# Kernel optimization log

Measured on AMD Instinct MI355X. Metric: run time of the kernel, lower is better.

The kernel has to match this reference:

```python
import jax, jax.numpy as jnp
import numpy as np

B, L, D, H = 2, 1024, 1024, 16
HEAD = D // H
BUCKETS = 256
MAX_REL = 512
ATT_SPAN = BUCKETS          # pos_ebd_size = position_buckets when buckets > 0
SCALE_FACTOR = 3            # 1 (content) + 1 (c2p) + 1 (p2c)


def _log_bucket(rel, bucket_size, max_position):
    """make_log_bucket_position: signed log-bucketed relative positions."""
    sign = jnp.sign(rel).astype(jnp.float32)
    mid = bucket_size // 2
    abs_pos = jnp.where((rel < mid) & (rel > -mid), mid - 1, jnp.abs(rel)).astype(jnp.float32)
    log_pos = jnp.ceil(jnp.log(abs_pos / mid) / np.float32(np.log((max_position - 1) / mid)) * (mid - 1)) + mid
    bucket = jnp.where(abs_pos <= mid, rel.astype(jnp.float32), log_pos * sign)
    return bucket.astype(jnp.int32)


def build_relative_position(q_len, k_len):
    rel = jnp.arange(q_len, dtype=jnp.int32)[:, None] - jnp.arange(k_len, dtype=jnp.int32)[None, :]
    return _log_bucket(rel, BUCKETS, MAX_REL)  # [q_len, k_len]


def setup_inputs() -> dict:
    key = jax.random.key(0)
    ks = jax.random.split(key, 6)
    w = 0.02  # typical init scale, keeps softmax well-conditioned
    return {
        "hidden_states": jax.random.normal(ks[0], (B, L, D), jnp.float32),
        "attention_mask": jnp.ones((B, L), jnp.int32),
        "rel_embeddings": jax.random.normal(ks[1], (2 * ATT_SPAN, D), jnp.float32) * w,
        "Wq": jax.random.normal(ks[2], (D, D), jnp.float32) * w,
        "bq": jnp.zeros((D,), jnp.float32),
        "Wk": jax.random.normal(ks[3], (D, D), jnp.float32) * w,
        "bk": jnp.zeros((D,), jnp.float32),
        "Wv": jax.random.normal(ks[4], (D, D), jnp.float32) * w,
        "bv": jnp.zeros((D,), jnp.float32),
    }


def reference(hidden_states, attention_mask, rel_embeddings, Wq, bq, Wk, bk, Wv, bv):
    Bn, Ln, Dn = hidden_states.shape

    def proj(x, W, b):  # Linear with bias, torch convention y = x W^T + b
        return x @ W.T + b

    def to_heads(x):  # [.., L, D] -> [.., H, L, HEAD]
        return x.reshape(*x.shape[:-1], H, HEAD).swapaxes(-3, -2)

    q = to_heads(proj(hidden_states, Wq, bq))  # [B,H,L,d]
    k = to_heads(proj(hidden_states, Wk, bk))
    v = to_heads(proj(hidden_states, Wv, bv))

    scale = jnp.sqrt(jnp.float32(HEAD * SCALE_FACTOR))
    scores = jnp.einsum('bhqd,bhkd->bhqk', q, k) / scale

    # disentangled relative-position bias (share_att_key=True -> reuse Wq/Wk)
    rel = build_relative_position(Ln, Ln)                     # [L,L] log-bucketed
    pos_k = proj(rel_embeddings, Wk, bk).reshape(2 * ATT_SPAN, H, HEAD)
    pos_q = proj(rel_embeddings, Wq, bq).reshape(2 * ATT_SPAN, H, HEAD)

    # c2p: Q . posK, gathered at (rel + span)
    c2p_att = jnp.einsum('bhqd,phd->bhqp', q, pos_k)          # [B,H,L,2S]
    c2p_idx = jnp.clip(rel + ATT_SPAN, 0, 2 * ATT_SPAN - 1)   # [L,L]
    c2p = jnp.take_along_axis(c2p_att, jnp.broadcast_to(c2p_idx[None, None], (Bn, H, Ln, Ln)), axis=-1)

    # p2c: K . posQ gathered at (-rel + span), then transposed to [q,k]
    p2c_att = jnp.einsum('bhkd,phd->bhkp', k, pos_q)          # [B,H,L,2S]
    p2c_idx = jnp.clip(-rel + ATT_SPAN, 0, 2 * ATT_SPAN - 1)
    p2c = jnp.take_along_axis(p2c_att, jnp.broadcast_to(p2c_idx[None, None], (Bn, H, Ln, Ln)), axis=-1)
    p2c = jnp.swapaxes(p2c, -1, -2)

    scores = scores + (c2p + p2c) / scale

    bias = jnp.where(attention_mask[:, None, None, :] > 0, 0.0, -1e9).astype(scores.dtype)
    probs = jax.nn.softmax(scores + bias, axis=-1)
    ctx = jnp.einsum('bhqk,bhkd->bhqd', probs, v)
    return ctx.swapaxes(1, 2).reshape(Bn, Ln, Dn)
```

## Files before the change

kernel.cpp:

```cpp
#include <hip/hip_runtime.h>


typedef short s8v __attribute__((ext_vector_type(8)));
typedef short s4v __attribute__((ext_vector_type(4)));
typedef float f32x4 __attribute__((ext_vector_type(4)));
typedef float f4v __attribute__((ext_vector_type(4)));

#define QK_SCALE 0.26864243f

__device__ __forceinline__ unsigned short f2bf(float f) {
  unsigned u = __builtin_bit_cast(unsigned, f);
  u += 0x7fffu + ((u >> 16) & 1u);
  return (unsigned short)(u >> 16);
}
__device__ __forceinline__ float bf2f(unsigned short h) {
  unsigned u = ((unsigned)h) << 16;
  return __builtin_bit_cast(float, u);
}

__device__ __forceinline__ void gload_lds16(const void* g, void* l) {
  __builtin_amdgcn_global_load_lds(
      (const __attribute__((address_space(1))) void*)g,
      (__attribute__((address_space(3))) void*)l, 16, 0, 0);
}

__global__ __launch_bounds__(256) void prep_kernel(
    const float* __restrict__ hidden, const float* __restrict__ rel,
    const float* __restrict__ Wq, const float* __restrict__ Wk,
    const float* __restrict__ Wv, const int* __restrict__ mask,
    short* __restrict__ Abf, short* __restrict__ Wbf,
    float* __restrict__ mbias, short* __restrict__ Tt) {
  int idx = blockIdx.x * 256 + threadIdx.x;
  const int NCONV = 1441792;
  if (idx < NCONV) {
    const float* src; short* dst; int off;
    if (idx < 524288) { src = hidden; dst = Abf; off = idx; }
    else if (idx < 655360) { src = rel; dst = Abf + 2048 * 1024; off = idx - 524288; }
    else {
      int j = idx - 655360;
      int w = j / 262144; off = j - w * 262144;
      src = (w == 0) ? Wq : (w == 1) ? Wk : Wv;
      dst = Wbf + w * 1048576;
    }
    f4v v = ((const f4v*)src)[off];
    s4v o;
    o[0] = (short)f2bf(v[0]); o[1] = (short)f2bf(v[1]);
    o[2] = (short)f2bf(v[2]); o[3] = (short)f2bf(v[3]);
    ((s4v*)dst)[off] = o;
  } else {
    int j = idx - NCONV;
    if (j < 2047) {
      int r = j - 1023;
      float fr = (float)r;
      float sign = (r > 0) ? 1.f : ((r < 0) ? -1.f : 0.f);
      float abs_pos = (r < 128 && r > -128) ? 127.f : fabsf(fr);
      const float logc = 1.3843393245589053f;
      float log_pos = ceilf(logf(abs_pos * (1.f / 128.f)) / logc * 127.f) + 128.f;
      float bucket = (abs_pos <= 128.f) ? fr : log_pos * sign;
      int bi = (int)bucket + 256;
      bi = bi < 0 ? 0 : (bi > 511 ? 511 : bi);
      Tt[j] = (short)bi;
    } else if (j < 4095) {
      int m = j - 2047;
      mbias[m] = (mask[m] > 0) ? 0.f : -1e9f;
    }
  }
}

__global__ __launch_bounds__(256) void gemm_qkv(
    const short* __restrict__ Abf, const short* __restrict__ Wbf,
    const float* __restrict__ bq, const float* __restrict__ bk,
    const float* __restrict__ bv,
    short* __restrict__ Qc, short* __restrict__ Kc, short* __restrict__ Vc) {
  __shared__ short As[128 * 64];
  __shared__ short Bs[128 * 64];
  int tid = threadIdx.x;
  int wid = tid >> 6, lane = tid & 63;
  int lr = lane & 15, lg = lane >> 4;
  int wr = wid >> 1, wc = wid & 1;
  int z = blockIdx.z;
  const short* W = Wbf + z * 1048576;
  const float* bias = (z == 0) ? bq : (z == 1) ? bk : bv;
  short* C = (z == 0) ? Qc : (z == 1) ? Kc : Vc;
  float scale = (z == 2) ? 1.f : QK_SCALE;
  int brow = blockIdx.y * 128;
  int bcol = blockIdx.x * 128;

  f32x4 acc[4][4];
  for (int i = 0; i < 4; i++)
    for (int j = 0; j < 4; j++) acc[i][j] = (f32x4){0.f, 0.f, 0.f, 0.f};

  for (int k0 = 0; k0 < 1024; k0 += 64) {
    for (int i = 0; i < 4; i++) {
      int n = i * 256 + wid * 64 + lane;
      const short* gA = Abf + (size_t)(brow + (n >> 3)) * 1024 + k0 + (n & 7) * 8;
      gload_lds16(gA, &As[(i * 256 + wid * 64) * 8]);
      const short* gB = W + (size_t)(bcol + (n >> 3)) * 1024 + k0 + (n & 7) * 8;
      gload_lds16(gB, &Bs[(i * 256 + wid * 64) * 8]);
    }
    __syncthreads();
    for (int ks = 0; ks < 2; ks++) {
      s8v af[4], bfv[4];
      for (int mi = 0; mi < 4; mi++)
        af[mi] = *(const s8v*)&As[(wr * 64 + mi * 16 + lr) * 64 + ks * 32 + lg * 8];
      for (int ni = 0; ni < 4; ni++)
        bfv[ni] = *(const s8v*)&Bs[(wc * 64 + ni * 16 + lr) * 64 + ks * 32 + lg * 8];
      for (int mi = 0; mi < 4; mi++)
        for (int ni = 0; ni < 4; ni++)
          acc[mi][ni] = __builtin_amdgcn_mfma_f32_16x16x32_bf16(
              af[mi], bfv[ni], acc[mi][ni], 0, 0, 0);
    }
    __syncthreads();
  }
  for (int mi = 0; mi < 4; mi++)
    for (int ni = 0; ni < 4; ni++) {
      int col = bcol + wc * 64 + ni * 16 + lr;
      float bb = bias[col];
      for (int r = 0; r < 4; r++) {
        int row = brow + wr * 64 + mi * 16 + lg * 4 + r;
        float v = (acc[mi][ni][r] + bb) * scale;
        C[(size_t)row * 1024 + col] = (short)f2bf(v);
      }
    }
}

__global__ __launch_bounds__(256) void pos_gemm(
    const short* __restrict__ Qc, const short* __restrict__ Kc,
    short* __restrict__ c2p, short* __restrict__ p2c) {
  __shared__ short As[128 * 64];
  __shared__ short Bs[128 * 64];
  int tid = threadIdx.x;
  int wid = tid >> 6, lane = tid & 63;
  int lr = lane & 15, lg = lane >> 4;
  int wr = wid >> 1, wc = wid & 1;
  int zz = blockIdx.z;
  int which = zz >> 5;
  int bh = zz & 31;
  int b = bh >> 4, h = bh & 15;
  const short* Arows = (which == 0) ? Qc : Kc;
  const short* Brows = (which == 0) ? Kc : Qc;
  short* Out = (which == 0) ? c2p : p2c;
  int mrow = blockIdx.y * 128;
  int ncol = blockIdx.x * 128;

  for (int i = 0; i < 4; i++) {
    int n = i * 256 + wid * 64 + lane;
    const short* gA = Arows + (size_t)(b * 1024 + mrow + (n >> 3)) * 1024 + h * 64 + (n & 7) * 8;
    gload_lds16(gA, &As[(i * 256 + wid * 64) * 8]);
    const short* gB = Brows + (size_t)(2048 + ncol + (n >> 3)) * 1024 + h * 64 + (n & 7) * 8;
    gload_lds16(gB, &Bs[(i * 256 + wid * 64) * 8]);
  }
  __syncthreads();

  f32x4 acc[4][4];
  for (int i = 0; i < 4; i++)
    for (int j = 0; j < 4; j++) acc[i][j] = (f32x4){0.f, 0.f, 0.f, 0.f};
  for (int ks = 0; ks < 2; ks++) {
    s8v af[4], bfv[4];
    for (int mi = 0; mi < 4; mi++)
      af[mi] = *(const s8v*)&As[(wr * 64 + mi * 16 + lr) * 64 + ks * 32 + lg * 8];
    for (int ni = 0; ni < 4; ni++)
      bfv[ni] = *(const s8v*)&Bs[(wc * 64 + ni * 16 + lr) * 64 + ks * 32 + lg * 8];
    for (int mi = 0; mi < 4; mi++)
      for (int ni = 0; ni < 4; ni++)
        acc[mi][ni] = __builtin_amdgcn_mfma_f32_16x16x32_bf16(
            af[mi], bfv[ni], acc[mi][ni], 0, 0, 0);
  }
  size_t base = (size_t)(b * 16 + h) * 1024;
  for (int mi = 0; mi < 4; mi++)
    for (int ni = 0; ni < 4; ni++)
      for (int r = 0; r < 4; r++) {
        int m = mrow + wr * 64 + mi * 16 + lg * 4 + r;
        int nn = ncol + wc * 64 + ni * 16 + lr;
        Out[(base + m) * 512 + nn] = (short)f2bf(acc[mi][ni][r]);
      }
}

__global__ __launch_bounds__(256) void transpose_v(
    const short* __restrict__ Vc, short* __restrict__ Vt) {
  __shared__ short TL[64 * 72];
  int tid = threadIdx.x;
  int lt = blockIdx.x, h = blockIdx.y, b = blockIdx.z;
  for (int i = 0; i < 2; i++) {
    int n = i * 256 + tid;
    int l = n >> 3, c = n & 7;
    s8v v = *(const s8v*)&Vc[(size_t)(b * 1024 + lt * 64 + l) * 1024 + h * 64 + c * 8];
    *(s8v*)&TL[l * 72 + c * 8] = v;
  }
  __syncthreads();
  for (int i = 0; i < 2; i++) {
    int m = i * 256 + tid;
    int d = m >> 3, c = m & 7;
    s8v o;
    for (int jj = 0; jj < 8; jj++) o[jj] = TL[(c * 8 + jj) * 72 + d];
    *(s8v*)&Vt[((size_t)(b * 16 + h) * 64 + d) * 1024 + lt * 64 + c * 8] = o;
  }
}

template <int NSPLIT>
__global__ __launch_bounds__(256) void attn_kernel(
    const short* __restrict__ Qc, const short* __restrict__ Kc,
    const short* __restrict__ Vt, const short* __restrict__ c2p,
    const short* __restrict__ p2c, const short* __restrict__ Tt,
    const float* __restrict__ mbias, float* __restrict__ Opart,
    float* __restrict__ dpart, float* __restrict__ out) {
  const int KSEG = 1024 / NSPLIT;
  const int TLN = 64 + KSEG - 1;
  __shared__ short Kl[64 * 64];
  __shared__ short Vl[64 * 64];
  __shared__ short Pl[4][16 * 72];
  __shared__ short Tl[TLN + 1];
  int tid = threadIdx.x;
  int wid = tid >> 6, lane = tid & 63;
  int lr = lane & 15, lg = lane >> 4;
  int qt = blockIdx.x, h = blockIdx.y, z = blockIdx.z;
  int b = (NSPLIT == 1) ? z : (z >> 2);
  int ks = (NSPLIT == 1) ? 0 : (z & 3);
  int k0seg = ks * KSEG;
  int q0 = qt * 64, qbase = q0 + wid * 16;
  size_t bh1024 = (size_t)(b * 16 + h) * 1024;

  for (int i = tid; i < TLN; i += 256) Tl[i] = Tt[(q0 - k0seg - (KSEG - 1) + 1023) + i];

  s8v aq[2];
  for (int s_ = 0; s_ < 2; s_++)
    aq[s_] = *(const s8v*)&Qc[(size_t)(b * 1024 + qbase + lr) * 1024 + h * 64 + s_ * 32 + lg * 8];

  f32x4 oacc[4];
  for (int n = 0; n < 4; n++) oacc[n] = (f32x4){0.f, 0.f, 0.f, 0.f};
  float dsum[4] = {0.f, 0.f, 0.f, 0.f};
  __syncthreads();

  for (int kt = k0seg; kt < k0seg + KSEG; kt += 64) {
    for (int i = 0; i < 2; i++) {
      int n = i * 256 + tid;
      int row = n >> 3, cb = n & 7, cbs = cb ^ (row & 7);
      s8v kv = *(const s8v*)&Kc[(size_t)(b * 1024 + kt + row) * 1024 + h * 64 + cb * 8];
      *(s8v*)&Kl[row * 64 + cbs * 8] = kv;
      s8v vv = *(const s8v*)&Vt[((size_t)(b * 16 + h) * 64 + row) * 1024 + kt + cb * 8];
      *(s8v*)&Vl[row * 64 + cbs * 8] = vv;
    }
    __syncthreads();

    f32x4 sacc[4];
    for (int n = 0; n < 4; n++) sacc[n] = (f32x4){0.f, 0.f, 0.f, 0.f};
    for (int s_ = 0; s_ < 2; s_++)
      for (int n = 0; n < 4; n++) {
        int row = n * 16 + lr, cb = s_ * 4 + lg, cbs = cb ^ (row & 7);
        s8v bk_ = *(const s8v*)&Kl[row * 64 + cbs * 8];
        sacc[n] = __builtin_amdgcn_mfma_f32_16x16x32_bf16(aq[s_], bk_, sacc[n], 0, 0, 0);
      }

    float c2v[4][4], p2v[4][4], mbv[4];
    int ktl = kt - k0seg;
    int jb = (qbase - q0) - ktl - lr + (KSEG - 1);
    for (int n = 0; n < 4; n++) {
      int k = kt + n * 16 + lr;
      mbv[n] = mbias[b * 1024 + k];
      size_t prow = (bh1024 + k) * 512;
      for (int r = 0; r < 4; r++) {
        int q = qbase + lg * 4 + r;
        int idx = Tl[jb + lg * 4 + r - n * 16];
        c2v[n][r] = bf2f((unsigned short)c2p[(bh1024 + q) * 512 + idx]);
        p2v[n][r] = bf2f((unsigned short)p2c[prow + idx]);
      }
    }
    for (int n = 0; n < 4; n++)
      for (int r = 0; r < 4; r++) {
        float p = __expf(sacc[n][r] + c2v[n][r] + p2v[n][r] + mbv[n]);
        dsum[r] += p;
        Pl[wid][(lg * 4 + r) * 72 + n * 16 + lr] = (short)f2bf(p);
      }
    __syncthreads();

    for (int s_ = 0; s_ < 2; s_++) {
      s8v ap = *(const s8v*)&Pl[wid][lr * 72 + s_ * 32 + lg * 8];
      for (int n = 0; n < 4; n++) {
        int row = n * 16 + lr, cb = s_ * 4 + lg, cbs = cb ^ (row & 7);
        s8v bv_ = *(const s8v*)&Vl[row * 64 + cbs * 8];
        oacc[n] = __builtin_amdgcn_mfma_f32_16x16x32_bf16(ap, bv_, oacc[n], 0, 0, 0);
      }
    }
    __syncthreads();
  }

  for (int m = 1; m < 16; m <<= 1)
    for (int r = 0; r < 4; r++) dsum[r] += __shfl_xor(dsum[r], m, 64);

  if (NSPLIT == 1) {
    for (int n = 0; n < 4; n++)
      for (int r = 0; r < 4; r++) {
        int q = qbase + lg * 4 + r;
        int d = n * 16 + lr;
        out[(size_t)(b * 1024 + q) * 1024 + h * 64 + d] = oacc[n][r] / dsum[r];
      }
  } else {
    size_t po = ((size_t)(z * 16 + h)) * 65536;
    for (int n = 0; n < 4; n++)
      for (int r = 0; r < 4; r++) {
        int q = qbase + lg * 4 + r;
        Opart[po + (size_t)q * 64 + n * 16 + lr] = oacc[n][r];
      }
    if (lr == 0)
      for (int r = 0; r < 4; r++)
        dpart[(z * 16 + h) * 1024 + qbase + lg * 4 + r] = dsum[r];
  }
}

__global__ __launch_bounds__(256) void combine_kernel(
    const float* __restrict__ Opart, const float* __restrict__ dpart,
    float* __restrict__ out) {
  int idx = blockIdx.x * 256 + threadIdx.x;
  int pos = idx * 4;
  int b = pos >> 20;
  int q = (pos >> 10) & 1023;
  int hd = pos & 1023;
  int h = hd >> 6, d = hd & 63;
  f4v s = (f4v){0.f, 0.f, 0.f, 0.f};
  float dn = 0.f;
  for (int ks = 0; ks < 4; ks++) {
    int zh = (b * 4 + ks) * 16 + h;
    s += *(const f4v*)&Opart[(size_t)zh * 65536 + q * 64 + d];
    dn += dpart[zh * 1024 + q];
  }
  f4v r = s / dn;
  *(f4v*)&out[pos] = r;
}

extern "C" void kernel_launch(void* const* d_in, const int* in_sizes, int n_in,
                              void* d_out, int out_size, void* d_ws, size_t ws_size,
                              hipStream_t stream) {
  (void)in_sizes; (void)n_in; (void)out_size;
  const float* hidden = (const float*)d_in[0];
  const int* mask = (const int*)d_in[1];
  const float* rel = (const float*)d_in[2];
  const float* Wq = (const float*)d_in[3];
  const float* bq = (const float*)d_in[4];
  const float* Wk = (const float*)d_in[5];
  const float* bk = (const float*)d_in[6];
  const float* Wv = (const float*)d_in[7];
  const float* bv = (const float*)d_in[8];
  float* out = (float*)d_out;

  char* w = (char*)d_ws;
  short* Abf = (short*)w; w += 2560 * 1024 * 2;
  short* Wbf = (short*)w; w += 3 * 1024 * 1024 * 2;
  short* Qc  = (short*)w; w += 2560 * 1024 * 2;
  short* Kc  = (short*)w; w += 2560 * 1024 * 2;
  short* Vc  = (short*)w; w += 2560 * 1024 * 2;
  short* Vt  = (short*)w; w += 2 * 16 * 64 * 1024 * 2;
  short* c2p = (short*)w; w += (size_t)2 * 16 * 1024 * 512 * 2;
  short* p2c = (short*)w; w += (size_t)2 * 16 * 1024 * 512 * 2;
  short* Tt  = (short*)w; w += 4096;
  float* mbias = (float*)w; w += 8192;
  float* Opart = (float*)w; w += (size_t)8 * 16 * 1024 * 64 * 4;
  float* dpart = (float*)w; w += 8 * 16 * 1024 * 4;
  size_t need = (size_t)(w - (char*)d_ws);

  prep_kernel<<<5648, 256, 0, stream>>>(hidden, rel, Wq, Wk, Wv, mask, Abf, Wbf, mbias, Tt);
  gemm_qkv<<<dim3(8, 20, 3), 256, 0, stream>>>(Abf, Wbf, bq, bk, bv, Qc, Kc, Vc);
  pos_gemm<<<dim3(4, 8, 64), 256, 0, stream>>>(Qc, Kc, c2p, p2c);
  transpose_v<<<dim3(16, 16, 2), 256, 0, stream>>>(Vc, Vt);
  if (ws_size >= need) {
    attn_kernel<4><<<dim3(16, 16, 8), 256, 0, stream>>>(Qc, Kc, Vt, c2p, p2c, Tt,
                                                        mbias, Opart, dpart, out);
    combine_kernel<<<2048, 256, 0, stream>>>(Opart, dpart, out);
  } else {
    attn_kernel<1><<<dim3(16, 16, 2), 256, 0, stream>>>(Qc, Kc, Vt, c2p, p2c, Tt,
                                                        mbias, Opart, dpart, out);
  }
}
```

Before: 140.8 us.

## Transpose c2p/p2c to position-major and stage the combined bias tile in LDS

The position GEMM now writes c2p and p2c transposed as [position][token], and the mask bias is folded into p2c there. Each K tile in the attention kernel gathers the relative-position bias along diagonals, so lanes read contiguous tokens for each bucket row. It adds c2p and p2c, stores the sum into an LDS tile, and the softmax step reads that tile instead of doing scattered global gathers. K/V global loads are also issued before the bias gather so their latency overlaps it, at the cost of extra LDS and a loop of 127 diagonal rows per tile with some wasted clamped loads.

Measured after the change: 198.3 us. 40.8% more time.

```diff
diff --git a/kernel.cpp b/kernel.cpp
--- a/kernel.cpp
+++ b/kernel.cpp
@@ -126,7 +126,8 @@
 
 __global__ __launch_bounds__(256) void pos_gemm(
     const short* __restrict__ Qc, const short* __restrict__ Kc,
-    short* __restrict__ c2p, short* __restrict__ p2c) {
+    const float* __restrict__ mbias,
+    short* __restrict__ c2pT, short* __restrict__ p2cT) {
   __shared__ short As[128 * 64];
   __shared__ short Bs[128 * 64];
   int tid = threadIdx.x;
@@ -139,15 +140,15 @@
   int b = bh >> 4, h = bh & 15;
   const short* Arows = (which == 0) ? Qc : Kc;
   const short* Brows = (which == 0) ? Kc : Qc;
-  short* Out = (which == 0) ? c2p : p2c;
+  short* Out = (which == 0) ? c2pT : p2cT;
   int mrow = blockIdx.y * 128;
-  int ncol = blockIdx.x * 128;
+  int pcol = blockIdx.x * 128;
 
   for (int i = 0; i < 4; i++) {
     int n = i * 256 + wid * 64 + lane;
     const short* gA = Arows + (size_t)(b * 1024 + mrow + (n >> 3)) * 1024 + h * 64 + (n & 7) * 8;
     gload_lds16(gA, &As[(i * 256 + wid * 64) * 8]);
-    const short* gB = Brows + (size_t)(2048 + ncol + (n >> 3)) * 1024 + h * 64 + (n & 7) * 8;
+    const short* gB = Brows + (size_t)(2048 + pcol + (n >> 3)) * 1024 + h * 64 + (n & 7) * 8;
     gload_lds16(gB, &Bs[(i * 256 + wid * 64) * 8]);
   }
   __syncthreads();
@@ -158,21 +159,23 @@
   for (int ks = 0; ks < 2; ks++) {
     s8v af[4], bfv[4];
     for (int mi = 0; mi < 4; mi++)
-      af[mi] = *(const s8v*)&As[(wr * 64 + mi * 16 + lr) * 64 + ks * 32 + lg * 8];
+      af[mi] = *(const s8v*)&Bs[(wr * 64 + mi * 16 + lr) * 64 + ks * 32 + lg * 8];
     for (int ni = 0; ni < 4; ni++)
-      bfv[ni] = *(const s8v*)&Bs[(wc * 64 + ni * 16 + lr) * 64 + ks * 32 + lg * 8];
+      bfv[ni] = *(const s8v*)&As[(wc * 64 + ni * 16 + lr) * 64 + ks * 32 + lg * 8];
     for (int mi = 0; mi < 4; mi++)
       for (int ni = 0; ni < 4; ni++)
         acc[mi][ni] = __builtin_amdgcn_mfma_f32_16x16x32_bf16(
             af[mi], bfv[ni], acc[mi][ni], 0, 0, 0);
   }
-  size_t base = (size_t)(b * 16 + h) * 1024;
+  size_t base = (size_t)(b * 16 + h) * 512;
   for (int mi = 0; mi < 4; mi++)
     for (int ni = 0; ni < 4; ni++)
       for (int r = 0; r < 4; r++) {
-        int m = mrow + wr * 64 + mi * 16 + lg * 4 + r;
-        int nn = ncol + wc * 64 + ni * 16 + lr;
-        Out[(base + m) * 512 + nn] = (short)f2bf(acc[mi][ni][r]);
+        int p = pcol + wr * 64 + mi * 16 + lg * 4 + r;
+        int m = mrow + wc * 64 + ni * 16 + lr;
+        float v = acc[mi][ni][r];
+        if (which == 1) v += mbias[b * 1024 + m];
+        Out[(base + p) * 1024 + m] = (short)f2bf(v);
       }
 }
 
@@ -200,15 +203,16 @@
 template <int NSPLIT>
 __global__ __launch_bounds__(256) void attn_kernel(
     const short* __restrict__ Qc, const short* __restrict__ Kc,
-    const short* __restrict__ Vt, const short* __restrict__ c2p,
-    const short* __restrict__ p2c, const short* __restrict__ Tt,
-    const float* __restrict__ mbias, float* __restrict__ Opart,
-    float* __restrict__ dpart, float* __restrict__ out) {
+    const short* __restrict__ Vt, const short* __restrict__ c2pT,
+    const short* __restrict__ p2cT, const short* __restrict__ Tt,
+    float* __restrict__ Opart, float* __restrict__ dpart,
+    float* __restrict__ out) {
   const int KSEG = 1024 / NSPLIT;
   const int TLN = 64 + KSEG - 1;
   __shared__ short Kl[64 * 64];
   __shared__ short Vl[64 * 64];
   __shared__ short Pl[4][16 * 72];
+  __shared__ short Bl[64 * 66];
   __shared__ short Tl[TLN + 1];
   int tid = threadIdx.x;
   int wid = tid >> 6, lane = tid & 63;
@@ -218,7 +222,7 @@
   int ks = (NSPLIT == 1) ? 0 : (z & 3);
   int k0seg = ks * KSEG;
   int q0 = qt * 64, qbase = q0 + wid * 16;
-  size_t bh1024 = (size_t)(b * 16 + h) * 1024;
+  size_t bh512 = (size_t)(b * 16 + h) * 512;
 
   for (int i = tid; i < TLN; i += 256) Tl[i] = Tt[(q0 - k0seg - (KSEG - 1) + 1023) + i];
 
@@ -232,13 +236,37 @@
   __syncthreads();
 
   for (int kt = k0seg; kt < k0seg + KSEG; kt += 64) {
+    s8v kvr[2], vvr[2];
+    for (int i = 0; i < 2; i++) {
+      int n = i * 256 + tid;
+      int row = n >> 3, cb = n & 7;
+      kvr[i] = *(const s8v*)&Kc[(size_t)(b * 1024 + kt + row) * 1024 + h * 64 + cb * 8];
+      vvr[i] = *(const s8v*)&Vt[((size_t)(b * 16 + h) * 64 + row) * 1024 + kt + cb * 8];
+    }
+
+    {
+      int ktl = kt - k0seg;
+      int tbase = (KSEG - 1) - ktl + 63;
+      int qq = lane;
+#pragma unroll 4
+      for (int j = wid; j < 127; j += 4) {
+        int rloc = j - 63;
+        int p = Tl[(KSEG - 1 - ktl) + rloc];
+        size_t rowb = (bh512 + p) * 1024;
+        int kk = qq - rloc;
+        int kkc = kk < 0 ? 0 : (kk > 63 ? 63 : kk);
+        float cv = bf2f((unsigned short)c2pT[rowb + q0 + qq]);
+        float pv = bf2f((unsigned short)p2cT[rowb + kt + kkc]);
+        if ((unsigned)kk < 64u) Bl[qq * 66 + kk] = (short)f2bf(cv + pv);
+      }
+      (void)tbase;
+    }
+
     for (int i = 0; i < 2; i++) {
       int n = i * 256 + tid;
       int row = n >> 3, cb = n & 7, cbs = cb ^ (row & 7);
-      s8v kv = *(const s8v*)&Kc[(size_t)(b * 1024 + kt + row) * 1024 + h * 64 + cb * 8];
-      *(s8v*)&Kl[row * 64 + cbs * 8] = kv;
-      s8v vv = *(const s8v*)&Vt[((size_t)(b * 16 + h) * 64 + row) * 1024 + kt + cb * 8];
-      *(s8v*)&Vl[row * 64 + cbs * 8] = vv;
+      *(s8v*)&Kl[row * 64 + cbs * 8] = kvr[i];
+      *(s8v*)&Vl[row * 64 + cbs * 8] = vvr[i];
     }
     __syncthreads();
 
@@ -251,23 +279,10 @@
         sacc[n] = __builtin_amdgcn_mfma_f32_16x16x32_bf16(aq[s_], bk_, sacc[n], 0, 0, 0);
       }
 
-    float c2v[4][4], p2v[4][4], mbv[4];
-    int ktl = kt - k0seg;
-    int jb = (qbase - q0) - ktl - lr + (KSEG - 1);
-    for (int n = 0; n < 4; n++) {
-      int k = kt + n * 16 + lr;
-      mbv[n] = mbias[b * 1024 + k];
-      size_t prow = (bh1024 + k) * 512;
-      for (int r = 0; r < 4; r++) {
-        int q = qbase + lg * 4 + r;
-        int idx = Tl[jb + lg * 4 + r - n * 16];
-        c2v[n][r] = bf2f((unsigned short)c2p[(bh1024 + q) * 512 + idx]);
-        p2v[n][r] = bf2f((unsigned short)p2c[prow + idx]);
-      }
-    }
     for (int n = 0; n < 4; n++)
       for (int r = 0; r < 4; r++) {
-        float p = __expf(sacc[n][r] + c2v[n][r] + p2v[n][r] + mbv[n]);
+        float bias = bf2f((unsigned short)Bl[(wid * 16 + lg * 4 + r) * 66 + n * 16 + lr]);
+        float p = __expf(sacc[n][r] + bias);
         dsum[r] += p;
         Pl[wid][(lg * 4 + r) * 72 + n * 16 + lr] = (short)f2bf(p);
       }
@@ -349,8 +364,8 @@
   short* Kc  = (short*)w; w += 2560 * 1024 * 2;
   short* Vc  = (short*)w; w += 2560 * 1024 * 2;
   short* Vt  = (short*)w; w += 2 * 16 * 64 * 1024 * 2;
-  short* c2p = (short*)w; w += (size_t)2 * 16 * 1024 * 512 * 2;
-  short* p2c = (short*)w; w += (size_t)2 * 16 * 1024 * 512 * 2;
+  short* c2pT = (short*)w; w += (size_t)2 * 16 * 512 * 1024 * 2;
+  short* p2cT = (short*)w; w += (size_t)2 * 16 * 512 * 1024 * 2;
   short* Tt  = (short*)w; w += 4096;
   float* mbias = (float*)w; w += 8192;
   float* Opart = (float*)w; w += (size_t)8 * 16 * 1024 * 64 * 4;
@@ -359,14 +374,14 @@
 
   prep_kernel<<<5648, 256, 0, stream>>>(hidden, rel, Wq, Wk, Wv, mask, Abf, Wbf, mbias, Tt);
   gemm_qkv<<<dim3(8, 20, 3), 256, 0, stream>>>(Abf, Wbf, bq, bk, bv, Qc, Kc, Vc);
-  pos_gemm<<<dim3(4, 8, 64), 256, 0, stream>>>(Qc, Kc, c2p, p2c);
+  pos_gemm<<<dim3(4, 8, 64), 256, 0, stream>>>(Qc, Kc, mbias, c2pT, p2cT);
   transpose_v<<<dim3(16, 16, 2), 256, 0, stream>>>(Vc, Vt);
   if (ws_size >= need) {
-    attn_kernel<4><<<dim3(16, 16, 8), 256, 0, stream>>>(Qc, Kc, Vt, c2p, p2c, Tt,
-                                                        mbias, Opart, dpart, out);
+    attn_kernel<4><<<dim3(16, 16, 8), 256, 0, stream>>>(Qc, Kc, Vt, c2pT, p2cT, Tt,
+                                                        Opart, dpart, out);
     combine_kernel<<<2048, 256, 0, stream>>>(Opart, dpart, out);
   } else {
-    attn_kernel<1><<<dim3(16, 16, 2), 256, 0, stream>>>(Qc, Kc, Vt, c2p, p2c, Tt,
-                                                        mbias, Opart, dpart, out);
-  }
-}
+    attn_kernel<1><<<dim3(16, 16, 2), 256, 0, stream>>>(Qc, Kc, Vt, c2pT, p2cT, Tt,
+                                                        Opart, dpart, out);
+  }
+}
```

## Stage c2p/p2c gathers through LDS and fold mask bias into p2c

Applied to the files above, without the earlier changes.

The attention kernel now gathers the c2p and p2c relative-position biases cooperatively into shared-memory tiles, with each lane walking one row so adjacent lanes read adjacent addresses. It then reads those tiles in the MFMA fragment layout, replacing scattered per-thread 2-byte global loads. The additive mask bias is folded into p2c during pos_gemm, which removes a per-tile mask load. K/V loads are issued into registers before the gather so their latency overlaps it, and the barrier between the per-wave P write and read is dropped. The cost is extra LDS use and bf16 rounding of the mask bias.

After: 218.1 us. +54.9%, slower.

```diff
diff --git a/kernel.cpp b/kernel.cpp
--- a/kernel.cpp
+++ b/kernel.cpp
@@ -126,6 +126,7 @@
 
 __global__ __launch_bounds__(256) void pos_gemm(
     const short* __restrict__ Qc, const short* __restrict__ Kc,
+    const float* __restrict__ mbias,
     short* __restrict__ c2p, short* __restrict__ p2c) {
   __shared__ short As[128 * 64];
   __shared__ short Bs[128 * 64];
@@ -172,7 +173,9 @@
       for (int r = 0; r < 4; r++) {
         int m = mrow + wr * 64 + mi * 16 + lg * 4 + r;
         int nn = ncol + wc * 64 + ni * 16 + lr;
-        Out[(base + m) * 512 + nn] = (short)f2bf(acc[mi][ni][r]);
+        float v = acc[mi][ni][r];
+        if (which == 1) v += mbias[b * 1024 + m];
+        Out[(base + m) * 512 + nn] = (short)f2bf(v);
       }
 }
 
@@ -202,13 +205,15 @@
     const short* __restrict__ Qc, const short* __restrict__ Kc,
     const short* __restrict__ Vt, const short* __restrict__ c2p,
     const short* __restrict__ p2c, const short* __restrict__ Tt,
-    const float* __restrict__ mbias, float* __restrict__ Opart,
-    float* __restrict__ dpart, float* __restrict__ out) {
+    float* __restrict__ Opart, float* __restrict__ dpart,
+    float* __restrict__ out) {
   const int KSEG = 1024 / NSPLIT;
   const int TLN = 64 + KSEG - 1;
   __shared__ short Kl[64 * 64];
   __shared__ short Vl[64 * 64];
   __shared__ short Pl[4][16 * 72];
+  __shared__ short Blc[64 * 66];
+  __shared__ short Blp[64 * 66];
   __shared__ short Tl[TLN + 1];
   int tid = threadIdx.x;
   int wid = tid >> 6, lane = tid & 63;
@@ -232,13 +237,33 @@
   __syncthreads();
 
   for (int kt = k0seg; kt < k0seg + KSEG; kt += 64) {
+    int ktl = kt - k0seg;
+    s8v kvr[2], vvr[2];
+    for (int i = 0; i < 2; i++) {
+      int n = i * 256 + tid;
+      int row = n >> 3, cb = n & 7;
+      kvr[i] = *(const s8v*)&Kc[(size_t)(b * 1024 + kt + row) * 1024 + h * 64 + cb * 8];
+      vvr[i] = *(const s8v*)&Vt[((size_t)(b * 16 + h) * 64 + row) * 1024 + kt + cb * 8];
+    }
+
+#pragma unroll
+    for (int ii = 0; ii < 16; ii++) {
+      int ql = wid * 16 + ii;
+      int idx = Tl[ql - lane - ktl + (KSEG - 1)];
+      Blc[ql * 66 + lane] = c2p[(bh1024 + q0 + ql) * 512 + idx];
+    }
+#pragma unroll
+    for (int ii = 0; ii < 16; ii++) {
+      int kl = wid * 16 + ii;
+      int idx = Tl[lane - kl - ktl + (KSEG - 1)];
+      Blp[kl * 66 + lane] = p2c[(bh1024 + kt + kl) * 512 + idx];
+    }
+
     for (int i = 0; i < 2; i++) {
       int n = i * 256 + tid;
       int row = n >> 3, cb = n & 7, cbs = cb ^ (row & 7);
-      s8v kv = *(const s8v*)&Kc[(size_t)(b * 1024 + kt + row) * 1024 + h * 64 + cb * 8];
-      *(s8v*)&Kl[row * 64 + cbs * 8] = kv;
-      s8v vv = *(const s8v*)&Vt[((size_t)(b * 16 + h) * 64 + row) * 1024 + kt + cb * 8];
-      *(s8v*)&Vl[row * 64 + cbs * 8] = vv;
+      *(s8v*)&Kl[row * 64 + cbs * 8] = kvr[i];
+      *(s8v*)&Vl[row * 64 + cbs * 8] = vvr[i];
     }
     __syncthreads();
 
@@ -251,27 +276,15 @@
         sacc[n] = __builtin_amdgcn_mfma_f32_16x16x32_bf16(aq[s_], bk_, sacc[n], 0, 0, 0);
       }
 
-    float c2v[4][4], p2v[4][4], mbv[4];
-    int ktl = kt - k0seg;
-    int jb = (qbase - q0) - ktl - lr + (KSEG - 1);
-    for (int n = 0; n < 4; n++) {
-      int k = kt + n * 16 + lr;
-      mbv[n] = mbias[b * 1024 + k];
-      size_t prow = (bh1024 + k) * 512;
-      for (int r = 0; r < 4; r++) {
-        int q = qbase + lg * 4 + r;
-        int idx = Tl[jb + lg * 4 + r - n * 16];
-        c2v[n][r] = bf2f((unsigned short)c2p[(bh1024 + q) * 512 + idx]);
-        p2v[n][r] = bf2f((unsigned short)p2c[prow + idx]);
-      }
-    }
     for (int n = 0; n < 4; n++)
       for (int r = 0; r < 4; r++) {
-        float p = __expf(sacc[n][r] + c2v[n][r] + p2v[n][r] + mbv[n]);
+        int qrow = wid * 16 + lg * 4 + r, kcol = n * 16 + lr;
+        float bias = bf2f((unsigned short)Blc[qrow * 66 + kcol]) +
+                     bf2f((unsigned short)Blp[kcol * 66 + qrow]);
+        float p = __expf(sacc[n][r] + bias);
         dsum[r] += p;
         Pl[wid][(lg * 4 + r) * 72 + n * 16 + lr] = (short)f2bf(p);
       }
-    __syncthreads();
 
     for (int s_ = 0; s_ < 2; s_++) {
       s8v ap = *(const s8v*)&Pl[wid][lr * 72 + s_ * 32 + lg * 8];
@@ -359,14 +372,14 @@
 
   prep_kernel<<<5648, 256, 0, stream>>>(hidden, rel, Wq, Wk, Wv, mask, Abf, Wbf, mbias, Tt);
   gemm_qkv<<<dim3(8, 20, 3), 256, 0, stream>>>(Abf, Wbf, bq, bk, bv, Qc, Kc, Vc);
-  pos_gemm<<<dim3(4, 8, 64), 256, 0, stream>>>(Qc, Kc, c2p, p2c);
+  pos_gemm<<<dim3(4, 8, 64), 256, 0, stream>>>(Qc, Kc, mbias, c2p, p2c);
   transpose_v<<<dim3(16, 16, 2), 256, 0, stream>>>(Vc, Vt);
   if (ws_size >= need) {
     attn_kernel<4><<<dim3(16, 16, 8), 256, 0, stream>>>(Qc, Kc, Vt, c2p, p2c, Tt,
-                                                        mbias, Opart, dpart, out);
+                                                        Opart, dpart, out);
     combine_kernel<<<2048, 256, 0, stream>>>(Opart, dpart, out);
   } else {
     attn_kernel<1><<<dim3(16, 16, 2), 256, 0, stream>>>(Qc, Kc, Vt, c2p, p2c, Tt,
-                                                        mbias, Opart, dpart, out);
-  }
-}
+                                                        Opart, dpart, out);
+  }
+}
```
